# Optimization experiments

Measured on AMD Instinct MI355X. Metric: run time of the kernel, lower is better.

## Reference

```python
import jax, jax.numpy as jnp
import numpy as np

N_NODES = 200000
N_EDGES = 12800000
C = 5  # channels
RADIUS = 0.05
CONSUME_RADIUS = RADIUS * 2
ACCEL_SCALE = 0.01
MAX_VEL = 0.1
CONSUME_EDGES_REQ = 3
EDGES_TO_STAY_ALIVE = 1
NEG_SLOPE = 0.2  # GATConv leaky_relu slope


def setup_inputs() -> dict:
    key = jax.random.key(0)
    ks = jax.random.split(key, 16)
    x = jax.random.normal(ks[0], (N_NODES, C), dtype=jnp.float32) * 0.1
    # column 4 is node type: 1 = cell, 0 = food
    is_cell = jax.random.bernoulli(ks[1], 0.9, (N_NODES,)).astype(jnp.float32)
    x = x.at[:, 4].set(is_cell)
    edge_index = jax.random.randint(ks[2], (2, N_EDGES), 0, N_NODES, dtype=jnp.int32)
    # edge_attr: [distance, is_cell_edge]
    dist = jax.random.uniform(ks[3], (N_EDGES,), dtype=jnp.float32) * 0.2
    cell_edge = jax.random.bernoulli(ks[4], 0.8, (N_EDGES,)).astype(jnp.float32)
    edge_attr = jnp.stack([dist, cell_edge], axis=1)
    s = 1.0 / np.sqrt(C)
    W = jax.random.normal(ks[5], (C, C), dtype=jnp.float32) * s        # GAT lin (shared src/dst)
    att_src = jax.random.normal(ks[6], (C,), dtype=jnp.float32) * s
    att_dst = jax.random.normal(ks[7], (C,), dtype=jnp.float32) * s
    We = jax.random.normal(ks[8], (2, C), dtype=jnp.float32) * 0.7      # lin_edge
    att_edge = jax.random.normal(ks[9], (C,), dtype=jnp.float32) * s
    gat_bias = jnp.zeros((C,), dtype=jnp.float32)
    W1 = jax.random.normal(ks[10], (C, C), dtype=jnp.float32) * s
    b1 = jnp.zeros((C,), dtype=jnp.float32)
    W2 = jax.random.normal(ks[11], (C, 2), dtype=jnp.float32) * s
    b2 = jnp.zeros((2,), dtype=jnp.float32)
    return {"x": x, "edge_index": edge_index, "edge_attr": edge_attr,
            "W": W, "att_src": att_src, "att_dst": att_dst, "We": We,
            "att_edge": att_edge, "gat_bias": gat_bias,
            "W1": W1, "b1": b1, "W2": W2, "b2": b2}


def _gat_conv(x, edge_index, edge_attr, W, att_src, att_dst, We, att_edge, gat_bias):
    # PyG GATConv, heads=1, edge_dim=2: softmax over incoming edges of each dst node
    n = x.shape[0]
    src, dst = edge_index[0], edge_index[1]
    hs = x @ W                                   # [N, C]
    a_src = hs @ att_src                         # [N]
    a_dst = hs @ att_dst                         # [N]
    a_e = (edge_attr @ We) @ att_edge            # [E]
    logits = jax.nn.leaky_relu(a_src[src] + a_dst[dst] + a_e, NEG_SLOPE)  # [E]
    m = jax.ops.segment_max(logits, dst, num_segments=n)                  # [N]
    ev = jnp.exp(logits - m[dst])
    denom = jax.ops.segment_sum(ev, dst, num_segments=n)                  # [N]
    alpha = ev / jnp.maximum(denom, 1e-16)[dst]
    out = jax.ops.segment_sum(hs[src] * alpha[:, None], dst, num_segments=n)
    return out + gat_bias


def reference(x, edge_index, edge_attr, W, att_src, att_dst, We, att_edge, gat_bias, W1, b1, W2, b2):
    n = x.shape[0]
    src = edge_index[0]
    # convolve: GAT -> MLP -> *2-1
    h = _gat_conv(x, edge_index, edge_attr, W, att_src, att_dst, We, att_edge, gat_bias)
    h = jax.nn.relu(jax.nn.relu(h @ W1 + b1) @ W2 + b2)
    h = h * 2.0 - 1.0                             # [N, 2]
    # only cells (type==1) accelerate
    food_mask = (x[:, 4] == 1).astype(jnp.float32)
    accel = h * ACCEL_SCALE * food_mask[:, None]
    velocity = jnp.clip(x[:, 2:4] + accel, -MAX_VEL, MAX_VEL)
    positions = x[:, :2] + velocity
    new_x = jnp.concatenate([positions, velocity, x[:, 4:]], axis=1)  # [N, 5]
    # border cost
    eps = 1e-6
    out_mask = (jnp.abs(positions) > 1).astype(jnp.float32)
    border_cost = jnp.sum(jnp.log(jnp.abs(positions) + eps) * out_mask)
    # consume-food mask: food nodes with >=3 close edges
    close = (edge_attr[:, 0] < CONSUME_RADIUS).astype(jnp.int32)
    close_cnt = jax.ops.segment_sum(close, src, num_segments=n)
    consumed = (x[:, 4] == 0) & (close_cnt >= CONSUME_EDGES_REQ)
    # island-cell mask: cells with < 1 cell-edge
    cell_e = (edge_attr[:, 1] == 1).astype(jnp.int32)
    cell_cnt = jax.ops.segment_sum(cell_e, src, num_segments=n)
    dead = (x[:, 4] == 1) & (cell_cnt < EDGES_TO_STAY_ALIVE)
    return (new_x, jnp.mean(jnp.abs(velocity), axis=0), border_cost,
            jnp.sum(consumed.astype(jnp.int32)), jnp.sum(dead.astype(jnp.int32)))
```

## Files before the change

kernel.cpp:

```cpp
#include <hip/hip_runtime.h>
#include <math.h>

#define NEG_SLOPE   0.2f
#define CONSUME_R   0.1f
#define ACCEL_SCALE 0.01f
#define MAX_VEL     0.1f

#define NBUCK  2048
#define TPB    512
#define EPT    16
#define EPB    (TPB*EPT)
#define MAXNPB 128
#define SMAX   6912
#define SCAP   1024

typedef float    v2f __attribute__((ext_vector_type(2)));
typedef unsigned v2u __attribute__((ext_vector_type(2)));

__device__ __forceinline__ unsigned bucket_of(unsigned v, unsigned npb, float inv_npb,
                                              unsigned* loc)
{
    unsigned b = (unsigned)((float)v * inv_npb);
    unsigned lo = b * npb;
    if (v < lo)            { --b; lo -= npb; }
    else if (v >= lo + npb){ ++b; lo += npb; }
    *loc = v - lo;
    return b;
}

__device__ __forceinline__ int slice_of(int blk, int NB)
{
    int q = NB >> 3, r = NB & 7;
    int xcd = blk & 7, idx = blk >> 3;
    return (xcd < r ? xcd * (q + 1) : r * (q + 1) + (xcd - r) * q) + idx;
}

__global__ __launch_bounds__(256) void k_pre(
    const float* __restrict__ x, const float* __restrict__ W,
    const float* __restrict__ att_src, const float* __restrict__ att_dst,
    uint4* __restrict__ npack, float* __restrict__ aD,
    int* __restrict__ pcur, float* __restrict__ scal, int n)
{
    int i = blockIdx.x * 256 + threadIdx.x;
    if (i >= n) return;
    if (i < 16) scal[i] = 0.f;
    if (i < 8 * NBUCK) pcur[i] = 0;
    float xr[5];
#pragma unroll
    for (int k = 0; k < 5; ++k) xr[k] = x[(size_t)i * 5 + k];
    float hs[5];
#pragma unroll
    for (int c = 0; c < 5; ++c) {
        float s = 0.f;
#pragma unroll
        for (int k = 0; k < 5; ++k) s += xr[k] * W[k * 5 + c];
        hs[c] = s;
    }
    float a_s = 0.f, a_d = 0.f;
#pragma unroll
    for (int c = 0; c < 5; ++c) { a_s += hs[c] * att_src[c]; a_d += hs[c] * att_dst[c]; }
    aD[i] = a_d;
    unsigned b[5];
#pragma unroll
    for (int c = 0; c < 5; ++c) {
        unsigned u = __float_as_uint(hs[c]);
        b[c] = (u + 0x7FFFu + ((u >> 16) & 1u)) >> 16;
    }
    npack[i] = make_uint4(b[0] | (b[1] << 16), b[2] | (b[3] << 16), b[4],
                          __float_as_uint(a_s));
}

__global__ __launch_bounds__(TPB) void k_hist(
    const int* __restrict__ dst, int* __restrict__ hist,
    int NB, int nE, unsigned npb, float inv_npb)
{
    __shared__ int hd[NBUCK];
    int t = threadIdx.x, blk = blockIdx.x;
    for (int j = t; j < NBUCK; j += TPB) hd[j] = 0;
    __syncthreads();
    int base = blk * EPB;
#pragma unroll 4
    for (int k = 0; k < EPT; ++k) {
        int e = base + k * TPB + t;
        if (e < nE) {
            unsigned loc;
            unsigned bd = bucket_of((unsigned)__builtin_nontemporal_load(dst + e),
                                    npb, inv_npb, &loc);
            atomicAdd(&hd[bd], 1);
        }
    }
    __syncthreads();
    for (int j = t; j < NBUCK; j += TPB) hist[(size_t)blk * NBUCK + j] = hd[j];
}

__global__ __launch_bounds__(256) void k_scanA(
    int* __restrict__ hist, int* __restrict__ rowtot, int NB)
{
    int b = blockIdx.x, t = threadIdx.x;
    __shared__ int ws4[4];
    __shared__ int carry;
    if (t == 0) carry = 0;
    __syncthreads();
    for (int base = 0; base < NB; base += 256) {
        int i = base + t;
        int v = (i < NB) ? hist[(size_t)i * NBUCK + b] : 0;
        int xv = v;
#pragma unroll
        for (int off = 1; off < 64; off <<= 1) {
            int y = __shfl_up(xv, off);
            if ((t & 63) >= off) xv += y;
        }
        if ((t & 63) == 63) ws4[t >> 6] = xv;
        __syncthreads();
        int add = 0;
        for (int w = 0; w < (t >> 6); ++w) add += ws4[w];
        int total = ws4[0] + ws4[1] + ws4[2] + ws4[3];
        if (i < NB) hist[(size_t)i * NBUCK + b] = carry + xv + add - v;
        __syncthreads();
        if (t == 0) carry += total;
        __syncthreads();
    }
    if (t == 0) rowtot[b] = carry;
}

__global__ __launch_bounds__(1024) void k_scanB(
    const int* __restrict__ rowtot, int* __restrict__ bbase)
{
    __shared__ int wsum[16], wex[16];
    int t = threadIdx.x;
    int a = rowtot[2 * t], b2 = rowtot[2 * t + 1];
    int v = a + b2;
    int xv = v;
#pragma unroll
    for (int off = 1; off < 64; off <<= 1) {
        int y = __shfl_up(xv, off);
        if ((t & 63) >= off) xv += y;
    }
    if ((t & 63) == 63) wsum[t >> 6] = xv;
    __syncthreads();
    if (t == 0) { int r = 0; for (int w = 0; w < 16; ++w) { wex[w] = r; r += wsum[w]; } }
    __syncthreads();
    int excl = xv - v + wex[t >> 6];
    bbase[2 * t] = excl;
    bbase[2 * t + 1] = excl + a;
    if (t == 1023) bbase[NBUCK] = excl + v;
}

__global__ __launch_bounds__(TPB) void k_scatter(
    const int* __restrict__ ei, const float* __restrict__ ea,
    const float* __restrict__ We, const float* __restrict__ att_edge,
    const int* __restrict__ hist, const int* __restrict__ bbase,
    unsigned* __restrict__ payD, unsigned short* __restrict__ payS,
    int* __restrict__ pcur, int NB, int nE, unsigned npb, float inv_npb)
{
    __shared__ int cD[NBUCK], cS[NBUCK], baseS[NBUCK], dirGl[NBUCK];
    int t = threadIdx.x;
    int sl = slice_of(blockIdx.x, NB);
    int xs = blockIdx.x & 7;
    for (int j = t; j < NBUCK; j += TPB) {
        cD[j] = 0; cS[j] = 0;
        dirGl[j] = bbase[j] + hist[(size_t)sl * NBUCK + j];
    }
    __syncthreads();

    float v0 = 0.f, v1 = 0.f;
#pragma unroll
    for (int c = 0; c < 5; ++c) { v0 += We[c] * att_edge[c]; v1 += We[5 + c] * att_edge[c]; }

    int base = sl * EPB;
    unsigned key[EPT], bb[EPT];
    float ae[EPT];

#pragma unroll
    for (int k = 0; k < EPT; ++k) {
        int e = base + k * TPB + t;
        bb[k] = 0;
        if (e < nE) {
            unsigned s = (unsigned)__builtin_nontemporal_load(ei + e);
            unsigned d = (unsigned)__builtin_nontemporal_load(ei + nE + e);
            v2f at = __builtin_nontemporal_load((const v2f*)ea + e);
            unsigned dloc, sloc;
            unsigned bd = bucket_of(d, npb, inv_npb, &dloc);
            unsigned bs = bucket_of(s, npb, inv_npb, &sloc);
            ae[k]  = at.x * v0 + at.y * v1;
            key[k] = s | (dloc << 18);
            bool close = at.x < CONSUME_R;
            bool cell  = (at.y == 1.0f);
            bb[k] = bd | (bs << 11) | (close ? (1u << 22) : 0u)
                       | (cell ? (1u << 23) : 0u) | (1u << 24);
            if (close || cell) atomicAdd(&cS[bs], 1);
        }
    }
    __syncthreads();

    for (int j = t; j < NBUCK; j += TPB) {
        int c = cS[j];
        baseS[j] = c ? atomicAdd(&pcur[xs * NBUCK + j], c) : 0;
        cS[j] = 0;
    }
    __syncthreads();

#pragma unroll
    for (int k = 0; k < EPT; ++k) {
        if (bb[k] & (1u << 24)) {
            unsigned bd = bb[k] & 0x7FFu;
            int r = atomicAdd(&cD[bd], 1);
            v2u rec; rec.x = key[k]; rec.y = __float_as_uint(ae[k]);
            ((v2u*)payD)[dirGl[bd] + r] = rec;
            if (bb[k] & 0xC00000u) {
                unsigned bs = (bb[k] >> 11) & 0x7FFu;
                unsigned sloc = (key[k] & 0x3FFFFu) - bs * npb;
                unsigned srec = sloc | ((bb[k] >> 22) & 1u) << 11 | ((bb[k] >> 23) & 1u) << 12;
                int r2 = atomicAdd(&cS[bs], 1);
                int p = baseS[bs] + r2;
                if (p < SCAP)
                    payS[((size_t)xs * NBUCK + bs) * SCAP + p] = (unsigned short)srec;
            }
        }
    }
}

__global__ __launch_bounds__(1024) void k_sortred(
    const unsigned* __restrict__ payD, const unsigned short* __restrict__ payS,
    const int* __restrict__ pcur, const int* __restrict__ bbase,
    const uint4* __restrict__ npack, const float* __restrict__ aD,
    const float* __restrict__ x,
    const float* __restrict__ gat_bias, const float* __restrict__ W1,
    const float* __restrict__ b1, const float* __restrict__ W2,
    const float* __restrict__ b2,
    float* __restrict__ out, float* __restrict__ scal,
    int n, int npb)
{
    __shared__ unsigned srt[SMAX * 2];
    __shared__ float accf[MAXNPB * 6];
    __shared__ float aDl[MAXNPB];
    __shared__ int cntL[MAXNPB], offL[MAXNPB], cnts[MAXNPB];
    __shared__ float sm[16][5];

    int b = blockIdx.x, t = threadIdx.x;
    int lo = bbase[b], hi = bbase[b + 1], span = hi - lo;
    int first = b * npb;
    int nodes = n - first; if (nodes > npb) nodes = npb; if (nodes < 0) nodes = 0;

    for (int j = t; j < npb; j += 1024) { cntL[j] = 0; cnts[j] = 0; }
    for (int j = t; j < npb * 6; j += 1024) accf[j] = 0.f;
    for (int j = t; j < nodes; j += 1024) aDl[j] = aD[first + j];
    __syncthreads();

    int grp = t >> 4, l16 = t & 15;

    if (span <= SMAX) {
        v2u recs[7];
#pragma unroll
        for (int k = 0; k < 7; ++k) {
            int idx = lo + k * 1024 + t;
            if (idx < hi) {
                recs[k] = __builtin_nontemporal_load((const v2u*)payD + idx);
                atomicAdd(&cntL[(recs[k].x >> 18) & 0x3FFu], 1);
            }
        }
        __syncthreads();
        if (t < 64) {
            int i0 = 2 * t, i1 = 2 * t + 1;
            int a0 = (i0 < npb) ? cntL[i0] : 0;
            int a1 = (i1 < npb) ? cntL[i1] : 0;
            int v = a0 + a1;
            int xv = v;
#pragma unroll
            for (int off = 1; off < 64; off <<= 1) {
                int y = __shfl_up(xv, off);
                if (t >= off) xv += y;
            }
            int ex = xv - v;
            if (i0 < npb) { offL[i0] = ex;      cntL[i0] = 0; }
            if (i1 < npb) { offL[i1] = ex + a0; cntL[i1] = 0; }
        }
        __syncthreads();
#pragma unroll
        for (int k = 0; k < 7; ++k) {
            int idx = lo + k * 1024 + t;
            if (idx < hi) {
                unsigned dl = (recs[k].x >> 18) & 0x3FFu;
                int r = atomicAdd(&cntL[dl], 1);
                int p = offL[dl] + r;
                srt[2 * p] = recs[k].x; srt[2 * p + 1] = recs[k].y;
            }
        }
        __syncthreads();
        for (int nd = grp; nd < nodes; nd += 64) {
            int s = offL[nd], e = s + cntL[nd];
            float s0 = 0.f, s1 = 0.f, s2 = 0.f, s3 = 0.f, s4 = 0.f, s5 = 0.f;
            for (int j = s + l16; j < e; j += 16) {
                unsigned w0 = srt[2 * j];
                float aev = __uint_as_float(srt[2 * j + 1]);
                uint4 hp = npack[w0 & 0x3FFFFu];
                float z = __uint_as_float(hp.w) + aev + aDl[nd];
                float l = z > 0.f ? z : NEG_SLOPE * z;
                float ev = __expf(l);
                s0 += ev * __uint_as_float(hp.x << 16);
                s1 += ev * __uint_as_float(hp.x & 0xFFFF0000u);
                s2 += ev * __uint_as_float(hp.y << 16);
                s3 += ev * __uint_as_float(hp.y & 0xFFFF0000u);
                s4 += ev * __uint_as_float(hp.z << 16);
                s5 += ev;
            }
#pragma unroll
            for (int m = 1; m < 16; m <<= 1) {
                s0 += __shfl_xor(s0, m);
                s1 += __shfl_xor(s1, m);
                s2 += __shfl_xor(s2, m);
                s3 += __shfl_xor(s3, m);
                s4 += __shfl_xor(s4, m);
                s5 += __shfl_xor(s5, m);
            }
            if (l16 == 0) {
                float* a = &accf[nd * 6];
                a[0] += s0; a[1] += s1; a[2] += s2; a[3] += s3; a[4] += s4; a[5] += s5;
            }
        }
    } else {
        for (int idx = lo + t; idx < hi; idx += 1024) {
            v2u rec = *((const v2u*)payD + idx);
            unsigned dl = (rec.x >> 18) & 0x3FFu;
            uint4 hp = npack[rec.x & 0x3FFFFu];
            float z = __uint_as_float(hp.w) + __uint_as_float(rec.y) + aDl[dl];
            float l = z > 0.f ? z : NEG_SLOPE * z;
            float ev = __expf(l);
            float* a = &accf[dl * 6];
            atomicAdd(a + 0, ev * __uint_as_float(hp.x << 16));
            atomicAdd(a + 1, ev * __uint_as_float(hp.x & 0xFFFF0000u));
            atomicAdd(a + 2, ev * __uint_as_float(hp.y << 16));
            atomicAdd(a + 3, ev * __uint_as_float(hp.y & 0xFFFF0000u));
            atomicAdd(a + 4, ev * __uint_as_float(hp.z << 16));
            atomicAdd(a + 5, ev);
        }
    }

    {
        int xsg = t >> 7, l128 = t & 127;
        int len = pcur[xsg * NBUCK + b];
        if (len > SCAP) len = SCAP;
        const unsigned short* run = payS + ((size_t)xsg * NBUCK + b) * SCAP;
        for (int j = l128; j < len; j += 128) {
            unsigned sr = run[j];
            int add = (int)((sr >> 11) & 1u) | (int)(((sr >> 12) & 1u) << 16);
            atomicAdd(&cnts[sr & 0x3FFu], add);
        }
    }
    __syncthreads();

    float part[5] = {0.f, 0.f, 0.f, 0.f, 0.f};
    if (t < nodes) {
        int i = first + t;
        const float* a = &accf[t * 6];
        float inv = 1.0f / fmaxf(a[5], 1e-16f);
        float h[5];
#pragma unroll
        for (int c = 0; c < 5; ++c) h[c] = a[c] * inv + gat_bias[c];
        float tt[5];
#pragma unroll
        for (int c = 0; c < 5; ++c) {
            float s = b1[c];
#pragma unroll
            for (int k = 0; k < 5; ++k) s += h[k] * W1[k * 5 + c];
            tt[c] = fmaxf(s, 0.f);
        }
        float u0 = b2[0], u1 = b2[1];
// ... 180 lines not shown
        for (int q = 0; q < 5; ++q) sm[wid][q] = part[q];
    __syncthreads();
    if (threadIdx.x == 0) {
#pragma unroll
        for (int q = 0; q < 5; ++q)
            unsafeAtomicAdd(scal + q, sm[0][q] + sm[1][q] + sm[2][q] + sm[3][q]);
    }
}

extern "C" void kernel_launch(void* const* d_in, const int* in_sizes, int n_in,
                              void* d_out, int out_size, void* d_ws, size_t ws_size,
                              hipStream_t stream)
{
    const float* x        = (const float*)d_in[0];
    const int*   ei       = (const int*)  d_in[1];
    const float* ea       = (const float*)d_in[2];
    const float* W        = (const float*)d_in[3];
    const float* att_src  = (const float*)d_in[4];
    const float* att_dst  = (const float*)d_in[5];
    const float* We       = (const float*)d_in[6];
    const float* att_edge = (const float*)d_in[7];
    const float* gat_bias = (const float*)d_in[8];
    const float* b1       = (const float*)d_in[10];
    const float* W1       = (const float*)d_in[9];
    const float* W2       = (const float*)d_in[11];
    const float* b2       = (const float*)d_in[12];

    int n  = in_sizes[0] / 5;
    int nE = in_sizes[1] / 2;

    int npb = (n + NBUCK - 1) / NBUCK;
    int NB = (nE + EPB - 1) / EPB;
    float inv_npb = 1.0f / (float)npb;

    size_t o = 0;
    auto alloc = [&](size_t bytes) { size_t r = o; o = (o + bytes + 63) & ~63ULL; return r; };
    size_t off_npack = alloc((size_t)n * 16);
    size_t off_aD    = alloc((size_t)n * 4);
    size_t off_hist  = alloc((size_t)NB * NBUCK * 4);
    size_t off_rtot  = alloc((size_t)NBUCK * 4);
    size_t off_bbase = alloc((size_t)(NBUCK + 1) * 4);
    size_t off_pcur  = alloc((size_t)8 * NBUCK * 4);
    size_t off_payS  = alloc((size_t)8 * NBUCK * SCAP * 2);
    size_t off_scal  = alloc(64);
    size_t off_payD  = alloc((size_t)nE * 8);
    size_t need = o;

    char* wsb = (char*)d_ws;
    bool ok_shape = (n < (1 << 18)) && (npb <= MAXNPB) && (NB >= 1);
    bool fast = ok_shape && (ws_size >= need);

    if (fast) {
        uint4*          npack = (uint4*)(wsb + off_npack);
        float*          aD    = (float*)(wsb + off_aD);
        int*            hist  = (int*)(wsb + off_hist);
        int*            rtot  = (int*)(wsb + off_rtot);
        int*            bbase = (int*)(wsb + off_bbase);
        int*            pcur  = (int*)(wsb + off_pcur);
        unsigned short* payS  = (unsigned short*)(wsb + off_payS);
        float*          scal  = (float*)(wsb + off_scal);
        unsigned*       payD  = (unsigned*)(wsb + off_payD);

        k_pre<<<(n + 255) / 256, 256, 0, stream>>>(x, W, att_src, att_dst, npack, aD,
                                                   pcur, scal, n);
        k_hist<<<NB, TPB, 0, stream>>>(ei + nE, hist, NB, nE, (unsigned)npb, inv_npb);
        k_scanA<<<NBUCK, 256, 0, stream>>>(hist, rtot, NB);
        k_scanB<<<1, 1024, 0, stream>>>(rtot, bbase);
        k_scatter<<<NB, TPB, 0, stream>>>(ei, ea, We, att_edge, hist, bbase,
                                          payD, payS, pcur, NB, nE, (unsigned)npb, inv_npb);
        k_sortred<<<NBUCK, 1024, 0, stream>>>(payD, payS, pcur, bbase, npack, aD, x,
                                              gat_bias, W1, b1, W2, b2,
                                              (float*)d_out, scal, n, npb);
        k_tail<<<1, 64, 0, stream>>>(scal, (float*)d_out, n);
    } else {
        float* ws    = (float*)d_ws;
        float* npk   = ws;
        float* acc   = ws + (size_t)n * 8;
        int*   cnt   = (int*)(acc + (size_t)n * 8);
        float* scal  = (float*)(cnt + n);
        size_t zbytes = ((size_t)n * 8 + (size_t)n + 8) * sizeof(float);
        hipMemsetAsync(acc, 0, zbytes, stream);
        k_node_pre_fb<<<(n + 255) / 256, 256, 0, stream>>>(x, W, att_src, att_dst, npk, n);
        k_edge_fb<<<(nE + 255) / 256, 256, 0, stream>>>(ei, ea, We, att_edge, npk,
                                                        acc, cnt, nE);
        k_final_fb<<<(n + 255) / 256, 256, 0, stream>>>(x, acc, cnt, gat_bias, W1, b1,
                                                        W2, b2, (float*)d_out, scal, n);
        k_tail<<<1, 64, 0, stream>>>(scal, (float*)d_out, n);
    }
}
```

Before: 689.9 us.

## Locally sort edges by dst bucket in LDS before coalesced payload scatter

The scatter kernel now builds a block-local counting sort: it counts edges per destination bucket, prefix-scans the counts in shared memory, and writes edge indices into an LDS sorted array. A final pass walks each bucket's contiguous range and writes payD records so that consecutive threads hit consecutive global addresses, replacing the random 8-byte scattered writes. The cost is a second read of ei/ea (non-temporal hints removed so they may hit cache), a 32KB LDS array that lowers occupancy, and extra barriers and a scan.

```diff
diff --git a/kernel.cpp b/kernel.cpp
--- a/kernel.cpp
+++ b/kernel.cpp
@@ -153,14 +153,14 @@
     unsigned* __restrict__ payD, unsigned short* __restrict__ payS,
     int* __restrict__ pcur, int NB, int nE, unsigned npb, float inv_npb)
 {
-    __shared__ int cD[NBUCK], cS[NBUCK], baseS[NBUCK], dirGl[NBUCK];
+    __shared__ unsigned srtL[EPB];
+    __shared__ int cD[NBUCK];
+    __shared__ int cS[NBUCK];
+    __shared__ int wsc[8], wex[8];
     int t = threadIdx.x;
     int sl = slice_of(blockIdx.x, NB);
     int xs = blockIdx.x & 7;
-    for (int j = t; j < NBUCK; j += TPB) {
-        cD[j] = 0; cS[j] = 0;
-        dirGl[j] = bbase[j] + hist[(size_t)sl * NBUCK + j];
-    }
+    for (int j = t; j < NBUCK; j += TPB) { cD[j] = 0; cS[j] = 0; }
     __syncthreads();
 
     float v0 = 0.f, v1 = 0.f;
@@ -168,54 +168,94 @@
     for (int c = 0; c < 5; ++c) { v0 += We[c] * att_edge[c]; v1 += We[5 + c] * att_edge[c]; }
 
     int base = sl * EPB;
-    unsigned key[EPT], bb[EPT];
-    float ae[EPT];
+    unsigned bb[EPT];
 
 #pragma unroll
     for (int k = 0; k < EPT; ++k) {
         int e = base + k * TPB + t;
         bb[k] = 0;
         if (e < nE) {
-            unsigned s = (unsigned)__builtin_nontemporal_load(ei + e);
-            unsigned d = (unsigned)__builtin_nontemporal_load(ei + nE + e);
-            v2f at = __builtin_nontemporal_load((const v2f*)ea + e);
+            unsigned s = (unsigned)ei[e];
+            unsigned d = (unsigned)ei[nE + e];
+            v2f at = *((const v2f*)ea + e);
             unsigned dloc, sloc;
             unsigned bd = bucket_of(d, npb, inv_npb, &dloc);
             unsigned bs = bucket_of(s, npb, inv_npb, &sloc);
-            ae[k]  = at.x * v0 + at.y * v1;
-            key[k] = s | (dloc << 18);
             bool close = at.x < CONSUME_R;
             bool cell  = (at.y == 1.0f);
-            bb[k] = bd | (bs << 11) | (close ? (1u << 22) : 0u)
-                       | (cell ? (1u << 23) : 0u) | (1u << 24);
+            bb[k] = bd | (dloc << 11) | (close ? (1u << 18) : 0u)
+                       | (cell ? (1u << 19) : 0u) | (1u << 20) | (bs << 21);
+            atomicAdd(&cD[bd], 1);
             if (close || cell) atomicAdd(&cS[bs], 1);
         }
     }
     __syncthreads();
 
+    {
+        int a0 = cD[4 * t], a1 = cD[4 * t + 1], a2 = cD[4 * t + 2], a3 = cD[4 * t + 3];
+        int lsum = a0 + a1 + a2 + a3;
+        int xv = lsum;
+#pragma unroll
+        for (int off = 1; off < 64; off <<= 1) {
+            int y = __shfl_up(xv, off);
+            if ((t & 63) >= off) xv += y;
+        }
+        if ((t & 63) == 63) wsc[t >> 6] = xv;
+        __syncthreads();
+        if (t == 0) { int r = 0; for (int w = 0; w < 8; ++w) { wex[w] = r; r += wsc[w]; } }
+        __syncthreads();
+        int b0 = xv - lsum + wex[t >> 6];
+        cD[4 * t]     = b0;
+        cD[4 * t + 1] = b0 + a0;
+        cD[4 * t + 2] = b0 + a0 + a1;
+        cD[4 * t + 3] = b0 + a0 + a1 + a2;
+    }
     for (int j = t; j < NBUCK; j += TPB) {
         int c = cS[j];
-        baseS[j] = c ? atomicAdd(&pcur[xs * NBUCK + j], c) : 0;
-        cS[j] = 0;
+        cS[j] = c ? atomicAdd(&pcur[xs * NBUCK + j], c) : 0;
     }
     __syncthreads();
 
 #pragma unroll
     for (int k = 0; k < EPT; ++k) {
-        if (bb[k] & (1u << 24)) {
+        if (bb[k] & (1u << 20)) {
             unsigned bd = bb[k] & 0x7FFu;
-            int r = atomicAdd(&cD[bd], 1);
-            v2u rec; rec.x = key[k]; rec.y = __float_as_uint(ae[k]);
-            ((v2u*)payD)[dirGl[bd] + r] = rec;
-            if (bb[k] & 0xC00000u) {
-                unsigned bs = (bb[k] >> 11) & 0x7FFu;
-                unsigned sloc = (key[k] & 0x3FFFFu) - bs * npb;
-                unsigned srec = sloc | ((bb[k] >> 22) & 1u) << 11 | ((bb[k] >> 23) & 1u) << 12;
-                int r2 = atomicAdd(&cS[bs], 1);
-                int p = baseS[bs] + r2;
-                if (p < SCAP)
-                    payS[((size_t)xs * NBUCK + bs) * SCAP + p] = (unsigned short)srec;
+            int p = atomicAdd(&cD[bd], 1);
+            srtL[p] = (unsigned)(k * TPB + t) | (((bb[k] >> 11) & 0x7Fu) << 13);
+            if (bb[k] & 0xC0000u) {
+                unsigned bs = bb[k] >> 21;
+                unsigned s = (unsigned)ei[base + k * TPB + t];
+                unsigned srec = (s - bs * npb) | ((bb[k] >> 18) & 1u) << 11
+                                              | ((bb[k] >> 19) & 1u) << 12;
+                int p2 = atomicAdd(&cS[bs], 1);
+                if (p2 < SCAP)
+                    payS[((size_t)xs * NBUCK + bs) * SCAP + p2] = (unsigned short)srec;
             }
+        }
+    }
+    __syncthreads();
+    for (int j = t; j < NBUCK; j += TPB) {
+        int basej = j ? cD[j - 1] : 0;
+        cS[j] = bbase[j] + hist[(size_t)sl * NBUCK + j] - basej;
+    }
+    __syncthreads();
+
+    int jj = t >> 2, sub = t & 3;
+#pragma unroll
+    for (int r = 0; r < NBUCK / (TPB / 4); ++r) {
+        int j = r * (TPB / 4) + jj;
+        int bs0 = j ? cD[j - 1] : 0;
+        int en0 = cD[j];
+        int adj = cS[j];
+        for (int p = bs0 + sub; p < en0; p += 4) {
+            unsigned rc = srtL[p];
+            int e = base + (int)(rc & 0x1FFFu);
+            unsigned s = (unsigned)ei[e];
+            v2f at = *((const v2f*)ea + e);
+            v2u rec;
+            rec.x = s | ((rc >> 13) << 18);
+            rec.y = __float_as_uint(at.x * v0 + at.y * v1);
+            ((v2u*)payD)[(size_t)adj + p] = rec;
         }
     }
 }
```

Result: slower. 815.0 us (+18.1%).

## Replace global histogram/scan sort with per-block coarse slab partition

Applied to the files above, without the earlier changes.

Removes the separate histogram and two scan kernels. Each scatter block now locally sorts its edges into 256 coarse destination buckets in shared memory, writes the slab out contiguously along with a per-block offset directory, and each reduction block reads its coarse bucket's segment from every slab, keeping only the edges for its fine bucket. This drops three launches and a full pass over the destination indices. The cost is that each slab segment is read by 8 fine-bucket blocks, about 8x redundant reads of the coarse data, plus many small strided reads per slab.

```diff
diff --git a/kernel.cpp b/kernel.cpp
--- a/kernel.cpp
+++ b/kernel.cpp
@@ -7,12 +7,14 @@
 #define MAX_VEL     0.1f
 
 #define NBUCK  2048
+#define NC     256
 #define TPB    512
 #define EPT    16
 #define EPB    (TPB*EPT)
 #define MAXNPB 128
 #define SMAX   6912
 #define SCAP   1024
+#define NBMAX  1600
 
 typedef float    v2f __attribute__((ext_vector_type(2)));
 typedef unsigned v2u __attribute__((ext_vector_type(2)));
@@ -70,97 +72,24 @@
                           __float_as_uint(a_s));
 }
 
-__global__ __launch_bounds__(TPB) void k_hist(
-    const int* __restrict__ dst, int* __restrict__ hist,
-    int NB, int nE, unsigned npb, float inv_npb)
-{
-    __shared__ int hd[NBUCK];
-    int t = threadIdx.x, blk = blockIdx.x;
-    for (int j = t; j < NBUCK; j += TPB) hd[j] = 0;
-    __syncthreads();
-    int base = blk * EPB;
-#pragma unroll 4
-    for (int k = 0; k < EPT; ++k) {
-        int e = base + k * TPB + t;
-        if (e < nE) {
-            unsigned loc;
-            unsigned bd = bucket_of((unsigned)__builtin_nontemporal_load(dst + e),
-                                    npb, inv_npb, &loc);
-            atomicAdd(&hd[bd], 1);
-        }
-    }
-    __syncthreads();
-    for (int j = t; j < NBUCK; j += TPB) hist[(size_t)blk * NBUCK + j] = hd[j];
-}
-
-__global__ __launch_bounds__(256) void k_scanA(
-    int* __restrict__ hist, int* __restrict__ rowtot, int NB)
-{
-    int b = blockIdx.x, t = threadIdx.x;
-    __shared__ int ws4[4];
-    __shared__ int carry;
-    if (t == 0) carry = 0;
-    __syncthreads();
-    for (int base = 0; base < NB; base += 256) {
-        int i = base + t;
-        int v = (i < NB) ? hist[(size_t)i * NBUCK + b] : 0;
-        int xv = v;
-#pragma unroll
-        for (int off = 1; off < 64; off <<= 1) {
-            int y = __shfl_up(xv, off);
-            if ((t & 63) >= off) xv += y;
-        }
-        if ((t & 63) == 63) ws4[t >> 6] = xv;
-        __syncthreads();
-        int add = 0;
-        for (int w = 0; w < (t >> 6); ++w) add += ws4[w];
-        int total = ws4[0] + ws4[1] + ws4[2] + ws4[3];
-        if (i < NB) hist[(size_t)i * NBUCK + b] = carry + xv + add - v;
-        __syncthreads();
-        if (t == 0) carry += total;
-        __syncthreads();
-    }
-    if (t == 0) rowtot[b] = carry;
-}
-
-__global__ __launch_bounds__(1024) void k_scanB(
-    const int* __restrict__ rowtot, int* __restrict__ bbase)
-{
-    __shared__ int wsum[16], wex[16];
-    int t = threadIdx.x;
-    int a = rowtot[2 * t], b2 = rowtot[2 * t + 1];
-    int v = a + b2;
-    int xv = v;
-#pragma unroll
-    for (int off = 1; off < 64; off <<= 1) {
-        int y = __shfl_up(xv, off);
-        if ((t & 63) >= off) xv += y;
-    }
-    if ((t & 63) == 63) wsum[t >> 6] = xv;
-    __syncthreads();
-    if (t == 0) { int r = 0; for (int w = 0; w < 16; ++w) { wex[w] = r; r += wsum[w]; } }
-    __syncthreads();
-    int excl = xv - v + wex[t >> 6];
-    bbase[2 * t] = excl;
-    bbase[2 * t + 1] = excl + a;
-    if (t == 1023) bbase[NBUCK] = excl + v;
-}
-
-__global__ __launch_bounds__(TPB) void k_scatter(
+__global__ __launch_bounds__(TPB) void k_scat1(
     const int* __restrict__ ei, const float* __restrict__ ea,
     const float* __restrict__ We, const float* __restrict__ att_edge,
-    const int* __restrict__ hist, const int* __restrict__ bbase,
-    unsigned* __restrict__ payD, unsigned short* __restrict__ payS,
-    int* __restrict__ pcur, int NB, int nE, unsigned npb, float inv_npb)
-{
-    __shared__ int cD[NBUCK], cS[NBUCK], baseS[NBUCK], dirGl[NBUCK];
+    unsigned* __restrict__ slabA, float* __restrict__ slabB,
+    unsigned short* __restrict__ dirC,
+    unsigned short* __restrict__ payS, int* __restrict__ pcur,
+    int NB, int nE, unsigned npb, float inv_npb,
+    unsigned npbC, float inv_npbC)
+{
+    __shared__ unsigned srtA[EPB];
+    __shared__ float    srtB[EPB];
+    __shared__ int cC[NC], cOffL[NC + 1], cS[NBUCK];
+    __shared__ int wscn[4];
     int t = threadIdx.x;
     int sl = slice_of(blockIdx.x, NB);
     int xs = blockIdx.x & 7;
-    for (int j = t; j < NBUCK; j += TPB) {
-        cD[j] = 0; cS[j] = 0;
-        dirGl[j] = bbase[j] + hist[(size_t)sl * NBUCK + j];
-    }
+    for (int j = t; j < NBUCK; j += TPB) cS[j] = 0;
+    if (t < NC) cC[t] = 0;
     __syncthreads();
 
     float v0 = 0.f, v1 = 0.f;
@@ -168,122 +97,170 @@
     for (int c = 0; c < 5; ++c) { v0 += We[c] * att_edge[c]; v1 += We[5 + c] * att_edge[c]; }
 
     int base = sl * EPB;
-    unsigned key[EPT], bb[EPT];
+    unsigned key[EPT], meta[EPT];
     float ae[EPT];
 
 #pragma unroll
     for (int k = 0; k < EPT; ++k) {
         int e = base + k * TPB + t;
-        bb[k] = 0;
+        meta[k] = 0;
         if (e < nE) {
             unsigned s = (unsigned)__builtin_nontemporal_load(ei + e);
             unsigned d = (unsigned)__builtin_nontemporal_load(ei + nE + e);
             v2f at = __builtin_nontemporal_load((const v2f*)ea + e);
-            unsigned dloc, sloc;
-            unsigned bd = bucket_of(d, npb, inv_npb, &dloc);
+            unsigned cloc, sloc;
+            unsigned cb = bucket_of(d, npbC, inv_npbC, &cloc);
             unsigned bs = bucket_of(s, npb, inv_npb, &sloc);
+            key[k] = s | (cloc << 18);
             ae[k]  = at.x * v0 + at.y * v1;
-            key[k] = s | (dloc << 18);
             bool close = at.x < CONSUME_R;
             bool cell  = (at.y == 1.0f);
-            bb[k] = bd | (bs << 11) | (close ? (1u << 22) : 0u)
-                       | (cell ? (1u << 23) : 0u) | (1u << 24);
+            meta[k] = cb | (bs << 8) | (close ? (1u << 19) : 0u)
+                         | (cell ? (1u << 20) : 0u) | (1u << 21);
+            atomicAdd(&cC[cb], 1);
             if (close || cell) atomicAdd(&cS[bs], 1);
         }
     }
     __syncthreads();
 
+    int v = 0, xv = 0;
+    if (t < NC) {
+        v = cC[t]; xv = v;
+#pragma unroll
+        for (int off = 1; off < 64; off <<= 1) {
+            int y = __shfl_up(xv, off);
+            if ((t & 63) >= off) xv += y;
+        }
+        if ((t & 63) == 63) wscn[t >> 6] = xv;
+    }
+    __syncthreads();
+    if (t < NC) {
+        int add = 0;
+        for (int w = 0; w < (t >> 6); ++w) add += wscn[w];
+        cOffL[t] = xv - v + add;
+        cC[t] = 0;
+        if (t == NC - 1) cOffL[NC] = xv + add;
+    }
     for (int j = t; j < NBUCK; j += TPB) {
         int c = cS[j];
-        baseS[j] = c ? atomicAdd(&pcur[xs * NBUCK + j], c) : 0;
-        cS[j] = 0;
+        cS[j] = c ? atomicAdd(&pcur[xs * NBUCK + j], c) : 0;
     }
     __syncthreads();
 
 #pragma unroll
     for (int k = 0; k < EPT; ++k) {
-        if (bb[k] & (1u << 24)) {
-            unsigned bd = bb[k] & 0x7FFu;
-            int r = atomicAdd(&cD[bd], 1);
-            v2u rec; rec.x = key[k]; rec.y = __float_as_uint(ae[k]);
-            ((v2u*)payD)[dirGl[bd] + r] = rec;
-            if (bb[k] & 0xC00000u) {
-                unsigned bs = (bb[k] >> 11) & 0x7FFu;
-                unsigned sloc = (key[k] & 0x3FFFFu) - bs * npb;
-                unsigned srec = sloc | ((bb[k] >> 22) & 1u) << 11 | ((bb[k] >> 23) & 1u) << 12;
-                int r2 = atomicAdd(&cS[bs], 1);
-                int p = baseS[bs] + r2;
-                if (p < SCAP)
-                    payS[((size_t)xs * NBUCK + bs) * SCAP + p] = (unsigned short)srec;
+        if (meta[k] & (1u << 21)) {
+            unsigned cb = meta[k] & 0xFFu;
+            int p = cOffL[cb] + atomicAdd(&cC[cb], 1);
+            srtA[p] = key[k];
+            srtB[p] = ae[k];
+            if (meta[k] & 0x180000u) {
+                unsigned bs = (meta[k] >> 8) & 0x7FFu;
+                unsigned s = key[k] & 0x3FFFFu;
+                unsigned srec = (s - bs * npb) | ((meta[k] >> 19) & 1u) << 11
+                                              | ((meta[k] >> 20) & 1u) << 12;
+                int p2 = atomicAdd(&cS[bs], 1);
+                if (p2 < SCAP)
+                    payS[((size_t)xs * NBUCK + bs) * SCAP + p2] = (unsigned short)srec;
             }
         }
     }
+    __syncthreads();
+
+    unsigned* gA = slabA + (size_t)sl * EPB;
+    float*    gB = slabB + (size_t)sl * EPB;
+#pragma unroll
+    for (int j = t; j < EPB; j += TPB) {
+        __builtin_nontemporal_store(srtA[j], gA + j);
+        __builtin_nontemporal_store(srtB[j], gB + j);
+    }
+    if (t <= NC) dirC[(size_t)t * NB + sl] = (unsigned short)cOffL[t];
 }
 
 __global__ __launch_bounds__(1024) void k_sortred(
-    const unsigned* __restrict__ payD, const unsigned short* __restrict__ payS,
-    const int* __restrict__ pcur, const int* __restrict__ bbase,
+    const unsigned* __restrict__ slabA, const float* __restrict__ slabB,
+    const unsigned short* __restrict__ dirC,
+    const unsigned short* __restrict__ payS, const int* __restrict__ pcur,
     const uint4* __restrict__ npack, const float* __restrict__ aD,
     const float* __restrict__ x,
     const float* __restrict__ gat_bias, const float* __restrict__ W1,
     const float* __restrict__ b1, const float* __restrict__ W2,
     const float* __restrict__ b2,
     float* __restrict__ out, float* __restrict__ scal,
-    int n, int npb)
+    int NB, int n, int npb, float inv_npb)
 {
     __shared__ unsigned srt[SMAX * 2];
+    __shared__ unsigned short dOf[NBMAX], dEn[NBMAX];
     __shared__ float accf[MAXNPB * 6];
     __shared__ float aDl[MAXNPB];
     __shared__ int cntL[MAXNPB], offL[MAXNPB], cnts[MAXNPB];
+    __shared__ int spanS;
     __shared__ float sm[16][5];
 
-    int b = blockIdx.x, t = threadIdx.x;
-    int lo = bbase[b], hi = bbase[b + 1], span = hi - lo;
+    int B = blockIdx.x, t = threadIdx.x;
+    int xcd = B & 7, idx = B >> 3;
+    int cb = xcd + 8 * (idx >> 3);
+    int f  = idx & 7;
+    int b  = cb * 8 + f;
     int first = b * npb;
     int nodes = n - first; if (nodes > npb) nodes = npb; if (nodes < 0) nodes = 0;
 
     for (int j = t; j < npb; j += 1024) { cntL[j] = 0; cnts[j] = 0; }
     for (int j = t; j < npb * 6; j += 1024) accf[j] = 0.f;
     for (int j = t; j < nodes; j += 1024) aDl[j] = aD[first + j];
+    for (int j = t; j < NB; j += 1024) {
+        dOf[j] = dirC[(size_t)cb * NB + j];
+        dEn[j] = dirC[(size_t)(cb + 1) * NB + j];
+    }
     __syncthreads();
 
     int grp = t >> 4, l16 = t & 15;
 
-    if (span <= SMAX) {
-        v2u recs[7];
-#pragma unroll
-        for (int k = 0; k < 7; ++k) {
-            int idx = lo + k * 1024 + t;
-            if (idx < hi) {
-                recs[k] = __builtin_nontemporal_load((const v2u*)payD + idx);
-                atomicAdd(&cntL[(recs[k].x >> 18) & 0x3FFu], 1);
-            }
-        }
-        __syncthreads();
-        if (t < 64) {
-            int i0 = 2 * t, i1 = 2 * t + 1;
-            int a0 = (i0 < npb) ? cntL[i0] : 0;
-            int a1 = (i1 < npb) ? cntL[i1] : 0;
-            int v = a0 + a1;
-            int xv = v;
-#pragma unroll
-            for (int off = 1; off < 64; off <<= 1) {
-                int y = __shfl_up(xv, off);
-                if (t >= off) xv += y;
-            }
-            int ex = xv - v;
-            if (i0 < npb) { offL[i0] = ex;      cntL[i0] = 0; }
-            if (i1 < npb) { offL[i1] = ex + a0; cntL[i1] = 0; }
-        }
-        __syncthreads();
-#pragma unroll
-        for (int k = 0; k < 7; ++k) {
-            int idx = lo + k * 1024 + t;
-            if (idx < hi) {
-                unsigned dl = (recs[k].x >> 18) & 0x3FFu;
-                int r = atomicAdd(&cntL[dl], 1);
-                int p = offL[dl] + r;
-                srt[2 * p] = recs[k].x; srt[2 * p + 1] = recs[k].y;
+    for (int sl = grp; sl < NB; sl += 64) {
+        int st = dOf[sl], en = dEn[sl];
+        const unsigned* pA = slabA + (size_t)sl * EPB;
+        for (int r = st + l16; r < en; r += 16) {
+            unsigned cloc = pA[r] >> 18;
+            unsigned dloc;
+            unsigned fl = bucket_of(cloc, npb, inv_npb, &dloc);
+            if (fl == (unsigned)f) atomicAdd(&cntL[dloc], 1);
+        }
+    }
+    __syncthreads();
+    if (t < 64) {
+        int i0 = 2 * t, i1 = 2 * t + 1;
+        int a0 = (i0 < npb) ? cntL[i0] : 0;
+        int a1 = (i1 < npb) ? cntL[i1] : 0;
+        int v = a0 + a1;
+        int xv = v;
+#pragma unroll
+        for (int off = 1; off < 64; off <<= 1) {
+            int y = __shfl_up(xv, off);
+            if (t >= off) xv += y;
+        }
+        int ex = xv - v;
+        if (i0 < npb) { offL[i0] = ex;      cntL[i0] = 0; }
+        if (i1 < npb) { offL[i1] = ex + a0; cntL[i1] = 0; }
+        if (t == 63) spanS = xv;
+    }
+    __syncthreads();
+
+    if (spanS <= SMAX) {
+        for (int sl = grp; sl < NB; sl += 64) {
+            int st = dOf[sl], en = dEn[sl];
+            const unsigned* pA = slabA + (size_t)sl * EPB;
+            const float*    pB = slabB + (size_t)sl * EPB;
+            for (int r = st + l16; r < en; r += 16) {
+                unsigned key = pA[r];
+                unsigned cloc = key >> 18;
+                unsigned dloc;
+                unsigned fl = bucket_of(cloc, npb, inv_npb, &dloc);
+                if (fl == (unsigned)f) {
+                    float aev = pB[r];
+                    int p = offL[dloc] + atomicAdd(&cntL[dloc], 1);
+                    srt[2 * p] = key & 0x3FFFFu;
+                    srt[2 * p + 1] = __float_as_uint(aev);
+                }
             }
         }
         __syncthreads();
@@ -293,7 +270,7 @@
             for (int j = s + l16; j < e; j += 16) {
                 unsigned w0 = srt[2 * j];
                 float aev = __uint_as_float(srt[2 * j + 1]);
-                uint4 hp = npack[w0 & 0x3FFFFu];
+                uint4 hp = npack[w0];
                 float z = __uint_as_float(hp.w) + aev + aDl[nd];
                 float l = z > 0.f ? z : NEG_SLOPE * z;
                 float ev = __expf(l);
@@ -319,20 +296,29 @@
             }
         }
     } else {
-        for (int idx = lo + t; idx < hi; idx += 1024) {
-            v2u rec = *((const v2u*)payD + idx);
-            unsigned dl = (rec.x >> 18) & 0x3FFu;
-            uint4 hp = npack[rec.x & 0x3FFFFu];
-            float z = __uint_as_float(hp.w) + __uint_as_float(rec.y) + aDl[dl];
-            float l = z > 0.f ? z : NEG_SLOPE * z;
-            float ev = __expf(l);
-            float* a = &accf[dl * 6];
-            atomicAdd(a + 0, ev * __uint_as_float(hp.x << 16));
-            atomicAdd(a + 1, ev * __uint_as_float(hp.x & 0xFFFF0000u));
-            atomicAdd(a + 2, ev * __uint_as_float(hp.y << 16));
-            atomicAdd(a + 3, ev * __uint_as_float(hp.y & 0xFFFF0000u));
-            atomicAdd(a + 4, ev * __uint_as_float(hp.z << 16));
-            atomicAdd(a + 5, ev);
+        for (int sl = grp; sl < NB; sl += 64) {
+            int st = dOf[sl], en = dEn[sl];
+            const unsigned* pA = slabA + (size_t)sl * EPB;
+            const float*    pB = slabB + (size_t)sl * EPB;
+            for (int r = st + l16; r < en; r += 16) {
+                unsigned key = pA[r];
+                unsigned cloc = key >> 18;
+                unsigned dloc;
+                unsigned fl = bucket_of(cloc, npb, inv_npb, &dloc);
+                if (fl == (unsigned)f) {
+                    uint4 hp = npack[key & 0x3FFFFu];
+                    float z = __uint_as_float(hp.w) + pB[r] + aDl[dloc];
+                    float l = z > 0.f ? z : NEG_SLOPE * z;
+                    float ev = __expf(l);
+                    float* a = &accf[dloc * 6];
+                    atomicAdd(a + 0, ev * __uint_as_float(hp.x << 16));
+                    atomicAdd(a + 1, ev * __uint_as_float(hp.x & 0xFFFF0000u));
+                    atomicAdd(a + 2, ev * __uint_as_float(hp.y << 16));
+                    atomicAdd(a + 3, ev * __uint_as_float(hp.y & 0xFFFF0000u));
+                    atomicAdd(a + 4, ev * __uint_as_float(hp.z << 16));
+                    atomicAdd(a + 5, ev);
+                }
+            }
         }
     }
 
@@ -579,45 +565,43 @@
     int npb = (n + NBUCK - 1) / NBUCK;
     int NB = (nE + EPB - 1) / EPB;
     float inv_npb = 1.0f / (float)npb;
+    unsigned npbC = (unsigned)npb * 8u;
+    float inv_npbC = 1.0f / (float)npbC;
 
     size_t o = 0;
     auto alloc = [&](size_t bytes) { size_t r = o; o = (o + bytes + 63) & ~63ULL; return r; };
     size_t off_npack = alloc((size_t)n * 16);
     size_t off_aD    = alloc((size_t)n * 4);
-    size_t off_hist  = alloc((size_t)NB * NBUCK * 4);
-    size_t off_rtot  = alloc((size_t)NBUCK * 4);
-    size_t off_bbase = alloc((size_t)(NBUCK + 1) * 4);
+    size_t off_dirC  = alloc((size_t)(NC + 1) * NB * 2);
     size_t off_pcur  = alloc((size_t)8 * NBUCK * 4);
     size_t off_payS  = alloc((size_t)8 * NBUCK * SCAP * 2);
     size_t off_scal  = alloc(64);
-    size_t off_payD  = alloc((size_t)nE * 8);
+    size_t off_slabA = alloc((size_t)NB * EPB * 4);
+    size_t off_slabB = alloc((size_t)NB * EPB * 4);
     size_t need = o;
 
     char* wsb = (char*)d_ws;
-    bool ok_shape = (n < (1 << 18)) && (npb <= MAXNPB) && (NB >= 1);
+    bool ok_shape = (n < (1 << 18)) && (npb <= MAXNPB) && (NB >= 1) && (NB <= NBMAX);
     bool fast = ok_shape && (ws_size >= need);
 
     if (fast) {
         uint4*          npack = (uint4*)(wsb + off_npack);
         float*          aD    = (float*)(wsb + off_aD);
-        int*            hist  = (int*)(wsb + off_hist);
-        int*            rtot  = (int*)(wsb + off_rtot);
-        int*            bbase = (int*)(wsb + off_bbase);
+        unsigned short* dirC  = (unsigned short*)(wsb + off_dirC);
         int*            pcur  = (int*)(wsb + off_pcur);
         unsigned short* payS  = (unsigned short*)(wsb + off_payS);
         float*          scal  = (float*)(wsb + off_scal);
-        unsigned*       payD  = (unsigned*)(wsb + off_payD);
+        unsigned*       slabA = (unsigned*)(wsb + off_slabA);
+        float*          slabB = (float*)(wsb + off_slabB);
 
         k_pre<<<(n + 255) / 256, 256, 0, stream>>>(x, W, att_src, att_dst, npack, aD,
                                                    pcur, scal, n);
-        k_hist<<<NB, TPB, 0, stream>>>(ei + nE, hist, NB, nE, (unsigned)npb, inv_npb);
-        k_scanA<<<NBUCK, 256, 0, stream>>>(hist, rtot, NB);
-        k_scanB<<<1, 1024, 0, stream>>>(rtot, bbase);
-        k_scatter<<<NB, TPB, 0, stream>>>(ei, ea, We, att_edge, hist, bbase,
-                                          payD, payS, pcur, NB, nE, (unsigned)npb, inv_npb);
-        k_sortred<<<NBUCK, 1024, 0, stream>>>(payD, payS, pcur, bbase, npack, aD, x,
-                                              gat_bias, W1, b1, W2, b2,
-                                              (float*)d_out, scal, n, npb);
+        k_scat1<<<NB, TPB, 0, stream>>>(ei, ea, We, att_edge, slabA, slabB, dirC,
+                                        payS, pcur, NB, nE, (unsigned)npb, inv_npb,
+                                        npbC, inv_npbC);
+        k_sortred<<<NBUCK, 1024, 0, stream>>>(slabA, slabB, dirC, payS, pcur,
+                                              npack, aD, x, gat_bias, W1, b1, W2, b2,
+                                              (float*)d_out, scal, NB, n, npb, inv_npb);
         k_tail<<<1, 64, 0, stream>>>(scal, (float*)d_out, n);
     } else {
         float* ws    = (float*)d_ws;
```

Result: slower. 819.6 us (+18.8%).

## Replace per-block histogram scan with atomic bucket reservation and padded sentinel slots

Applied to the files above, without the earlier changes.

Drops the per-block histogram array and its column scan kernel. Bucket totals are now accumulated with global atomics, padded per block to a multiple of up to 8. The scatter kernel reserves each block's destination range through atomic cursors, and fills the padding slots with sentinel records. This removes a kernel launch and the large hist read/write traffic, and lets scatter blocks write aligned chunks. The cost is extra sentinel records that the sort-reduce kernel must read and skip, nondeterministic edge order within buckets, and the need for a larger workspace.

```diff
diff --git a/kernel.cpp b/kernel.cpp
--- a/kernel.cpp
+++ b/kernel.cpp
@@ -13,6 +13,7 @@
 #define MAXNPB 128
 #define SMAX   6912
 #define SCAP   1024
+#define SENT   0xFFFFFFFFu
 
 typedef float    v2f __attribute__((ext_vector_type(2)));
 typedef unsigned v2u __attribute__((ext_vector_type(2)));
@@ -28,23 +29,17 @@
     return b;
 }
 
-__device__ __forceinline__ int slice_of(int blk, int NB)
-{
-    int q = NB >> 3, r = NB & 7;
-    int xcd = blk & 7, idx = blk >> 3;
-    return (xcd < r ? xcd * (q + 1) : r * (q + 1) + (xcd - r) * q) + idx;
-}
-
 __global__ __launch_bounds__(256) void k_pre(
     const float* __restrict__ x, const float* __restrict__ W,
     const float* __restrict__ att_src, const float* __restrict__ att_dst,
     uint4* __restrict__ npack, float* __restrict__ aD,
-    int* __restrict__ pcur, float* __restrict__ scal, int n)
+    int* __restrict__ pcur, int* __restrict__ rtot8,
+    float* __restrict__ scal, int n)
 {
     int i = blockIdx.x * 256 + threadIdx.x;
     if (i >= n) return;
     if (i < 16) scal[i] = 0.f;
-    if (i < 8 * NBUCK) pcur[i] = 0;
+    if (i < 8 * NBUCK) { pcur[i] = 0; rtot8[i] = 0; }
     float xr[5];
 #pragma unroll
     for (int k = 0; k < 5; ++k) xr[k] = x[(size_t)i * 5 + k];
@@ -70,9 +65,9 @@
                           __float_as_uint(a_s));
 }
 
-__global__ __launch_bounds__(TPB) void k_hist(
-    const int* __restrict__ dst, int* __restrict__ hist,
-    int NB, int nE, unsigned npb, float inv_npb)
+__global__ __launch_bounds__(TPB) void k_cnt(
+    const int* __restrict__ dst, int* __restrict__ rtot8,
+    int nE, unsigned npb, float inv_npb, int padm)
 {
     __shared__ int hd[NBUCK];
     int t = threadIdx.x, blk = blockIdx.x;
@@ -90,45 +85,24 @@
         }
     }
     __syncthreads();
-    for (int j = t; j < NBUCK; j += TPB) hist[(size_t)blk * NBUCK + j] = hd[j];
-}
-
-__global__ __launch_bounds__(256) void k_scanA(
-    int* __restrict__ hist, int* __restrict__ rowtot, int NB)
-{
-    int b = blockIdx.x, t = threadIdx.x;
-    __shared__ int ws4[4];
-    __shared__ int carry;
-    if (t == 0) carry = 0;
-    __syncthreads();
-    for (int base = 0; base < NB; base += 256) {
-        int i = base + t;
-        int v = (i < NB) ? hist[(size_t)i * NBUCK + b] : 0;
-        int xv = v;
-#pragma unroll
-        for (int off = 1; off < 64; off <<= 1) {
-            int y = __shfl_up(xv, off);
-            if ((t & 63) >= off) xv += y;
-        }
-        if ((t & 63) == 63) ws4[t >> 6] = xv;
-        __syncthreads();
-        int add = 0;
-        for (int w = 0; w < (t >> 6); ++w) add += ws4[w];
-        int total = ws4[0] + ws4[1] + ws4[2] + ws4[3];
-        if (i < NB) hist[(size_t)i * NBUCK + b] = carry + xv + add - v;
-        __syncthreads();
-        if (t == 0) carry += total;
-        __syncthreads();
-    }
-    if (t == 0) rowtot[b] = carry;
+    int xs = blk & 7;
+    for (int j = t; j < NBUCK; j += TPB) {
+        int c = hd[j];
+        if (c) atomicAdd(&rtot8[xs * NBUCK + j], (c + padm) & ~padm);
+    }
 }
 
 __global__ __launch_bounds__(1024) void k_scanB(
-    const int* __restrict__ rowtot, int* __restrict__ bbase)
+    const int* __restrict__ rtot8, int* __restrict__ bbase, int* __restrict__ dcur)
 {
     __shared__ int wsum[16], wex[16];
     int t = threadIdx.x;
-    int a = rowtot[2 * t], b2 = rowtot[2 * t + 1];
+    int a = 0, b2 = 0;
+#pragma unroll
+    for (int xq = 0; xq < 8; ++xq) {
+        a  += rtot8[xq * NBUCK + 2 * t];
+        b2 += rtot8[xq * NBUCK + 2 * t + 1];
+    }
     int v = a + b2;
     int xv = v;
 #pragma unroll
@@ -141,33 +115,30 @@
     if (t == 0) { int r = 0; for (int w = 0; w < 16; ++w) { wex[w] = r; r += wsum[w]; } }
     __syncthreads();
     int excl = xv - v + wex[t >> 6];
-    bbase[2 * t] = excl;
-    bbase[2 * t + 1] = excl + a;
+    bbase[2 * t] = excl;        dcur[2 * t] = excl;
+    bbase[2 * t + 1] = excl + a; dcur[2 * t + 1] = excl + a;
     if (t == 1023) bbase[NBUCK] = excl + v;
 }
 
 __global__ __launch_bounds__(TPB) void k_scatter(
     const int* __restrict__ ei, const float* __restrict__ ea,
     const float* __restrict__ We, const float* __restrict__ att_edge,
-    const int* __restrict__ hist, const int* __restrict__ bbase,
     unsigned* __restrict__ payD, unsigned short* __restrict__ payS,
-    int* __restrict__ pcur, int NB, int nE, unsigned npb, float inv_npb)
-{
-    __shared__ int cD[NBUCK], cS[NBUCK], baseS[NBUCK], dirGl[NBUCK];
-    int t = threadIdx.x;
-    int sl = slice_of(blockIdx.x, NB);
-    int xs = blockIdx.x & 7;
-    for (int j = t; j < NBUCK; j += TPB) {
-        cD[j] = 0; cS[j] = 0;
-        dirGl[j] = bbase[j] + hist[(size_t)sl * NBUCK + j];
-    }
+    int* __restrict__ pcur, int* __restrict__ dcur,
+    int nE, unsigned npb, float inv_npb, int padm, long long dcap)
+{
+    __shared__ int cD[NBUCK], cS[NBUCK];
+    __shared__ unsigned dirGl[NBUCK];
+    int t = threadIdx.x, blk = blockIdx.x;
+    int xs = blk & 7;
+    for (int j = t; j < NBUCK; j += TPB) { cD[j] = 0; cS[j] = 0; }
     __syncthreads();
 
     float v0 = 0.f, v1 = 0.f;
 #pragma unroll
     for (int c = 0; c < 5; ++c) { v0 += We[c] * att_edge[c]; v1 += We[5 + c] * att_edge[c]; }
 
-    int base = sl * EPB;
+    int base = blk * EPB;
     unsigned key[EPT], bb[EPT];
     float ae[EPT];
 
@@ -188,15 +159,19 @@
             bool cell  = (at.y == 1.0f);
             bb[k] = bd | (bs << 11) | (close ? (1u << 22) : 0u)
                        | (cell ? (1u << 23) : 0u) | (1u << 24);
+            atomicAdd(&cD[bd], 1);
             if (close || cell) atomicAdd(&cS[bs], 1);
         }
     }
     __syncthreads();
 
     for (int j = t; j < NBUCK; j += TPB) {
-        int c = cS[j];
-        baseS[j] = c ? atomicAdd(&pcur[xs * NBUCK + j], c) : 0;
-        cS[j] = 0;
+        int c = cD[j];
+        int padc = (c + padm) & ~padm;
+        dirGl[j] = padc ? (unsigned)atomicAdd(&dcur[j], padc) : 0u;
+        cD[j] = 0;
+        int f = cS[j];
+        cS[j] = f ? atomicAdd(&pcur[xs * NBUCK + j], f) : 0;
     }
     __syncthreads();
 
@@ -205,16 +180,32 @@
         if (bb[k] & (1u << 24)) {
             unsigned bd = bb[k] & 0x7FFu;
             int r = atomicAdd(&cD[bd], 1);
-            v2u rec; rec.x = key[k]; rec.y = __float_as_uint(ae[k]);
-            ((v2u*)payD)[dirGl[bd] + r] = rec;
+            long long pidx = (long long)dirGl[bd] + r;
+            if (pidx < dcap) {
+                v2u rec; rec.x = key[k]; rec.y = __float_as_uint(ae[k]);
+                ((v2u*)payD)[pidx] = rec;
+            }
             if (bb[k] & 0xC00000u) {
                 unsigned bs = (bb[k] >> 11) & 0x7FFu;
                 unsigned sloc = (key[k] & 0x3FFFFu) - bs * npb;
                 unsigned srec = sloc | ((bb[k] >> 22) & 1u) << 11 | ((bb[k] >> 23) & 1u) << 12;
-                int r2 = atomicAdd(&cS[bs], 1);
-                int p = baseS[bs] + r2;
-                if (p < SCAP)
-                    payS[((size_t)xs * NBUCK + bs) * SCAP + p] = (unsigned short)srec;
+                int p2 = atomicAdd(&cS[bs], 1);
+                if (p2 < SCAP)
+                    payS[((size_t)xs * NBUCK + bs) * SCAP + p2] = (unsigned short)srec;
+            }
+        }
+    }
+    __syncthreads();
+
+    for (int j = t; j < NBUCK; j += TPB) {
+        int real = cD[j];
+        int padc = (real + padm) & ~padm;
+        unsigned b0 = dirGl[j];
+        for (int p = real; p < padc; ++p) {
+            long long pidx = (long long)b0 + p;
+            if (pidx < dcap) {
+                v2u rec; rec.x = SENT; rec.y = 0u;
+                ((v2u*)payD)[pidx] = rec;
             }
         }
     }
@@ -229,16 +220,18 @@
     const float* __restrict__ b1, const float* __restrict__ W2,
     const float* __restrict__ b2,
     float* __restrict__ out, float* __restrict__ scal,
-    int n, int npb)
+    int n, int npb, long long dcap)
 {
     __shared__ unsigned srt[SMAX * 2];
     __shared__ float accf[MAXNPB * 6];
     __shared__ float aDl[MAXNPB];
     __shared__ int cntL[MAXNPB], offL[MAXNPB], cnts[MAXNPB];
+    __shared__ int spanS;
     __shared__ float sm[16][5];
 
     int b = blockIdx.x, t = threadIdx.x;
-    int lo = bbase[b], hi = bbase[b + 1], span = hi - lo;
+    int lo = bbase[b], hi = bbase[b + 1];
+    if ((long long)hi > dcap) hi = (int)dcap;
     int first = b * npb;
     int nodes = n - first; if (nodes > npb) nodes = npb; if (nodes < 0) nodes = 0;
 
@@ -249,41 +242,37 @@
 
     int grp = t >> 4, l16 = t & 15;
 
-    if (span <= SMAX) {
-        v2u recs[7];
-#pragma unroll
-        for (int k = 0; k < 7; ++k) {
-            int idx = lo + k * 1024 + t;
-            if (idx < hi) {
-                recs[k] = __builtin_nontemporal_load((const v2u*)payD + idx);
-                atomicAdd(&cntL[(recs[k].x >> 18) & 0x3FFu], 1);
-            }
-        }
-        __syncthreads();
-        if (t < 64) {
-            int i0 = 2 * t, i1 = 2 * t + 1;
-            int a0 = (i0 < npb) ? cntL[i0] : 0;
-            int a1 = (i1 < npb) ? cntL[i1] : 0;
-            int v = a0 + a1;
-            int xv = v;
-#pragma unroll
-            for (int off = 1; off < 64; off <<= 1) {
-                int y = __shfl_up(xv, off);
-                if (t >= off) xv += y;
-            }
-            int ex = xv - v;
-            if (i0 < npb) { offL[i0] = ex;      cntL[i0] = 0; }
-            if (i1 < npb) { offL[i1] = ex + a0; cntL[i1] = 0; }
-        }
-        __syncthreads();
-#pragma unroll
-        for (int k = 0; k < 7; ++k) {
-            int idx = lo + k * 1024 + t;
-            if (idx < hi) {
-                unsigned dl = (recs[k].x >> 18) & 0x3FFu;
+    for (int idx = lo + t; idx < hi; idx += 1024) {
+        v2u rec = *((const v2u*)payD + idx);
+        if (rec.x != SENT) atomicAdd(&cntL[(rec.x >> 18) & 0x3FFu], 1);
+    }
+    __syncthreads();
+    if (t < 64) {
+        int i0 = 2 * t, i1 = 2 * t + 1;
+        int a0 = (i0 < npb) ? cntL[i0] : 0;
+        int a1 = (i1 < npb) ? cntL[i1] : 0;
+        int v = a0 + a1;
+        int xv = v;
+#pragma unroll
+        for (int off = 1; off < 64; off <<= 1) {
+            int y = __shfl_up(xv, off);
+            if (t >= off) xv += y;
+        }
+        int ex = xv - v;
+        if (i0 < npb) { offL[i0] = ex;      cntL[i0] = 0; }
+        if (i1 < npb) { offL[i1] = ex + a0; cntL[i1] = 0; }
+        if (t == 63) spanS = xv;
+    }
+    __syncthreads();
+
+    if (spanS <= SMAX) {
+        for (int idx = lo + t; idx < hi; idx += 1024) {
+            v2u rec = *((const v2u*)payD + idx);
+            if (rec.x != SENT) {
+                unsigned dl = (rec.x >> 18) & 0x3FFu;
                 int r = atomicAdd(&cntL[dl], 1);
                 int p = offL[dl] + r;
-                srt[2 * p] = recs[k].x; srt[2 * p + 1] = recs[k].y;
+                srt[2 * p] = rec.x; srt[2 * p + 1] = rec.y;
             }
         }
         __syncthreads();
@@ -321,6 +310,7 @@
     } else {
         for (int idx = lo + t; idx < hi; idx += 1024) {
             v2u rec = *((const v2u*)payD + idx);
+            if (rec.x == SENT) continue;
             unsigned dl = (rec.x >> 18) & 0x3FFu;
             uint4 hp = npack[rec.x & 0x3FFFFu];
             float z = __uint_as_float(hp.w) + __uint_as_float(rec.y) + aDl[dl];
@@ -584,14 +574,21 @@
     auto alloc = [&](size_t bytes) { size_t r = o; o = (o + bytes + 63) & ~63ULL; return r; };
     size_t off_npack = alloc((size_t)n * 16);
     size_t off_aD    = alloc((size_t)n * 4);
-    size_t off_hist  = alloc((size_t)NB * NBUCK * 4);
-    size_t off_rtot  = alloc((size_t)NBUCK * 4);
+    size_t off_rtot8 = alloc((size_t)8 * NBUCK * 4);
     size_t off_bbase = alloc((size_t)(NBUCK + 1) * 4);
+    size_t off_dcur  = alloc((size_t)NBUCK * 4);
     size_t off_pcur  = alloc((size_t)8 * NBUCK * 4);
     size_t off_payS  = alloc((size_t)8 * NBUCK * SCAP * 2);
     size_t off_scal  = alloc(64);
-    size_t off_payD  = alloc((size_t)nE * 8);
-    size_t need = o;
+    size_t off_payD  = alloc(0);
+
+    int pad = 1;
+    for (int p = 8; p >= 2; p >>= 1) {
+        size_t cap = (size_t)nE + (size_t)(p - 1) * NB * NBUCK;
+        if (off_payD + cap * 8 <= ws_size) { pad = p; break; }
+    }
+    size_t cap1 = (size_t)nE + (size_t)(pad - 1) * NB * NBUCK;
+    size_t need = off_payD + cap1 * 8;
 
     char* wsb = (char*)d_ws;
     bool ok_shape = (n < (1 << 18)) && (npb <= MAXNPB) && (NB >= 1);
@@ -600,24 +597,26 @@
     if (fast) {
         uint4*          npack = (uint4*)(wsb + off_npack);
         float*          aD    = (float*)(wsb + off_aD);
-        int*            hist  = (int*)(wsb + off_hist);
-        int*            rtot  = (int*)(wsb + off_rtot);
+        int*            rtot8 = (int*)(wsb + off_rtot8);
         int*            bbase = (int*)(wsb + off_bbase);
+        int*            dcur  = (int*)(wsb + off_dcur);
         int*            pcur  = (int*)(wsb + off_pcur);
         unsigned short* payS  = (unsigned short*)(wsb + off_payS);
         float*          scal  = (float*)(wsb + off_scal);
         unsigned*       payD  = (unsigned*)(wsb + off_payD);
+        int padm = pad - 1;
+        long long dcap = (long long)cap1;
 
         k_pre<<<(n + 255) / 256, 256, 0, stream>>>(x, W, att_src, att_dst, npack, aD,
-                                                   pcur, scal, n);
-        k_hist<<<NB, TPB, 0, stream>>>(ei + nE, hist, NB, nE, (unsigned)npb, inv_npb);
-        k_scanA<<<NBUCK, 256, 0, stream>>>(hist, rtot, NB);
-        k_scanB<<<1, 1024, 0, stream>>>(rtot, bbase);
-        k_scatter<<<NB, TPB, 0, stream>>>(ei, ea, We, att_edge, hist, bbase,
-                                          payD, payS, pcur, NB, nE, (unsigned)npb, inv_npb);
+                                                   pcur, rtot8, scal, n);
+        k_cnt<<<NB, TPB, 0, stream>>>(ei + nE, rtot8, nE, (unsigned)npb, inv_npb, padm);
+        k_scanB<<<1, 1024, 0, stream>>>(rtot8, bbase, dcur);
+        k_scatter<<<NB, TPB, 0, stream>>>(ei, ea, We, att_edge, payD, payS,
+                                          pcur, dcur, nE, (unsigned)npb, inv_npb,
+                                          padm, dcap);
         k_sortred<<<NBUCK, 1024, 0, stream>>>(payD, payS, pcur, bbase, npack, aD, x,
                                               gat_bias, W1, b1, W2, b2,
-                                              (float*)d_out, scal, n, npb);
+                                              (float*)d_out, scal, n, npb, dcap);
         k_tail<<<1, 64, 0, stream>>>(scal, (float*)d_out, n);
     } else {
         float* ws    = (float*)d_ws;
```

Measured after the change: 753.2 us. 9.2% more time.
